# Optimization experiments

Measured on AMD Instinct MI355X. Metric: run time of the kernel, lower is better.

## Reference

```python
import jax, jax.numpy as jnp
import numpy as np

TEMPERATURE = 0.5
EPS = 1e-12  # F.normalize eps


def setup_inputs() -> dict:
    key = jax.random.key(0)
    z = jax.random.normal(key, (2048, 8, 256), dtype=jnp.float32)
    return {"z": z}


def reference(z):
    B, D = z.shape[0], z.shape[1]
    z = z.reshape(B, D, -1)  # [B, D, F]
    # F.normalize along features
    norm = jnp.linalg.norm(z, axis=-1, keepdims=True)
    zn = z / jnp.maximum(norm, EPS)

    # Positive term: per sample b, sim among D views -> [B, D, D], off-diagonal sum
    sim_pos = jnp.exp(jnp.einsum('bdf,bef->bde', zn, zn) / TEMPERATURE)
    eye_d = jnp.eye(D, dtype=bool)
    pos = jnp.sum(jnp.where(eye_d[None], 0.0, sim_pos), axis=(1, 2))  # [B]

    # Negative term: per view d, sim among B samples -> [D, B, B], row-wise off-diag mean, summed over views
    sim_neg = jnp.exp(jnp.einsum('bdf,cdf->dbc', zn, zn) / TEMPERATURE)
    eye_b = jnp.eye(B, dtype=bool)
    neg = jnp.sum(jnp.where(eye_b[None], 0.0, sim_neg), axis=-1) / (B - 1)  # [D, B]
    neg = jnp.sum(neg, axis=0)  # [B]

    logits = pos / (pos + neg)  # [B]
    # torch CrossEntropyLoss(reduction='sum') with 1-D input [C] and float target ones(C):
    # loss = -sum_c target_c * log_softmax(logits)_c = -sum(log_softmax(logits))
    error = -jnp.sum(jax.nn.log_softmax(logits))
    return error / B
```

## Files before the change

### kernel.cpp

```cpp
#include <hip/hip_runtime.h>
#include <hip/hip_bf16.h>

#define B_N 2048
#define D_V 8
#define F_D 256
#define TILE 128
#define BC 64
#define LSTR 264

#define SCALE_F 1.69864364f

#if defined(__has_builtin)
#  if __has_builtin(__builtin_amdgcn_exp2f)
#    define EXP2F(x) __builtin_amdgcn_exp2f(x)
#  else
#    define EXP2F(x) exp2f(x)
#  endif
#else
#  define EXP2F(x) exp2f(x)
#endif

typedef __attribute__((ext_vector_type(8))) short short8;
typedef __attribute__((ext_vector_type(4))) float floatx4;

__device__ inline unsigned short f2bf(float f) {
    __hip_bfloat16 h = __float2bfloat16(f);
    return *reinterpret_cast<unsigned short*>(&h);
}

__device__ inline float wave_reduce_sum(float v) {
    #pragma unroll
    for (int off = 1; off < 64; off <<= 1)
        v += __shfl_xor(v, off, 64);
    return v;
}

__global__ void norm_kernel(const float* __restrict__ z,
                            unsigned short* __restrict__ zn,
                            float* __restrict__ ns8) {
    int gid = blockIdx.x * blockDim.x + threadIdx.x;
    if (gid < D_V * B_N) ns8[gid] = 0.0f;
    int wave = gid >> 6;
    int lane = threadIdx.x & 63;
    const float4* zp = (const float4*)(z + (size_t)wave * F_D);
    float4 v = zp[lane];
    float ss = v.x * v.x + v.y * v.y + v.z * v.z + v.w * v.w;
    ss = wave_reduce_sum(ss);
    float inv = SCALE_F / fmaxf(sqrtf(ss), 1e-12f);
    int b = wave >> 3, d = wave & 7;
    unsigned short* op = zn + (size_t)d * (B_N * F_D) + (size_t)b * F_D + lane * 4;
    ushort4 o;
    o.x = f2bf(v.x * inv);
    o.y = f2bf(v.y * inv);
    o.z = f2bf(v.z * inv);
    o.w = f2bf(v.w * inv);
    *(ushort4*)op = o;
}

__global__ void pos_kernel(const unsigned short* __restrict__ zn,
                           float* __restrict__ pos) {
    int gw = (blockIdx.x * blockDim.x + threadIdx.x) >> 6;
    int lane = threadIdx.x & 63;
    int q = lane >> 4, li = lane & 15;
    int s0 = gw * 2;
    int b = s0 + (li >> 3), d = li & 7;
    const unsigned short* rowp = zn + (size_t)d * (B_N * F_D) + (size_t)b * F_D;
    short8 a[8];
    #pragma unroll
    for (int kk = 0; kk < 8; kk++)
        a[kk] = *(const short8*)(rowp + kk * 32 + q * 8);
    floatx4 acc = {0.f, 0.f, 0.f, 0.f};
    #pragma unroll
    for (int kk = 0; kk < 8; kk++)
        acc = __builtin_amdgcn_mfma_f32_16x16x32_bf16(a[kk], a[kk], acc, 0, 0, 0);
    float p0 = 0.f, p1 = 0.f;
    #pragma unroll
    for (int r = 0; r < 4; r++) {
        int row = q * 4 + r, col = li;
        bool same_sample = (row >> 3) == (col >> 3);
        if (same_sample && row != col) {
            float e = EXP2F(acc[r]);
            if (row < 8) p0 += e; else p1 += e;
        }
    }
    p0 = wave_reduce_sum(p0);
    p1 = wave_reduce_sum(p1);
    if (lane == 0) { pos[s0] = p0; pos[s0 + 1] = p1; }
}

__global__ __launch_bounds__(256)
void neg_kernel(const unsigned short* __restrict__ zn,
                float* __restrict__ ns8) {
    __shared__ __align__(16) unsigned short Bs[BC * LSTR];
    const int bid = blockIdx.x;
    const int d = bid & 7;
    int trem = bid >> 3;
    int i = 0;
    while (trem >= 16 - i) { trem -= 16 - i; ++i; }
    const int j = i + trem;
    const bool diag = (i == j);
    const unsigned short* Z = zn + (size_t)d * (B_N * F_D);
    int tid = threadIdx.x, w = tid >> 6, lane = tid & 63;
    int q = lane >> 4, li = lane & 15;
    int r0 = i * TILE + w * 32;

    short8 a[2][8];
    #pragma unroll
    for (int s = 0; s < 2; s++)
        #pragma unroll
        for (int kk = 0; kk < 8; kk++)
            a[s][kk] = *(const short8*)(Z + (size_t)(r0 + s * 16 + li) * F_D + kk * 32 + q * 8);

    float rs[2][4];
    #pragma unroll
    for (int s = 0; s < 2; s++)
        #pragma unroll
        for (int r = 0; r < 4; r++) rs[s][r] = 0.f;
    float cs[8];

    #pragma unroll
    for (int stage = 0; stage < 2; ++stage) {
        int c0 = j * TILE + stage * BC;
        __syncthreads();
        #pragma unroll
        for (int it = 0; it < 8; ++it) {
            int idx = it * 256 + tid;
            int row = idx >> 5, kc = idx & 31;
            *(short8*)(&Bs[row * LSTR + kc * 8]) =
                *(const short8*)(Z + (size_t)(c0 + row) * F_D + kc * 8);
        }
        __syncthreads();
        #pragma unroll
        for (int ct = 0; ct < 4; ++ct) {
            const unsigned short* bp = &Bs[(ct * 16 + li) * LSTR + q * 8];
            floatx4 acc[2];
            acc[0] = (floatx4){0.f, 0.f, 0.f, 0.f};
            acc[1] = (floatx4){0.f, 0.f, 0.f, 0.f};
            #pragma unroll
            for (int kk = 0; kk < 8; kk++) {
                short8 bf = *(const short8*)(bp + kk * 32);
                acc[0] = __builtin_amdgcn_mfma_f32_16x16x32_bf16(a[0][kk], bf, acc[0], 0, 0, 0);
                acc[1] = __builtin_amdgcn_mfma_f32_16x16x32_bf16(a[1][kk], bf, acc[1], 0, 0, 0);
            }
            int gcol = c0 + ct * 16 + li;
            float csum = 0.f;
            #pragma unroll
            for (int s = 0; s < 2; s++) {
                #pragma unroll
                for (int r = 0; r < 4; r++) {
                    float e = EXP2F(acc[s][r]);
                    if (diag) {
                        int grow = r0 + s * 16 + q * 4 + r;
                        if (grow == gcol) e = 0.f;
                    }
                    rs[s][r] += e;
                    csum += e;
                }
            }
            cs[stage * 4 + ct] = csum;
        }
    }

    #pragma unroll
    for (int off = 1; off < 16; off <<= 1)
        #pragma unroll
        for (int s = 0; s < 2; s++)
            #pragma unroll
            for (int r = 0; r < 4; r++)
                rs[s][r] += __shfl_xor(rs[s][r], off, 64);
    {
        float rv = 0.f;
        #pragma unroll
        for (int s = 0; s < 2; s++)
            #pragma unroll
            for (int r = 0; r < 4; r++)
                if (li == s * 4 + r) rv = rs[s][r];
        if (li < 8)
            atomicAdd(&ns8[d * B_N + r0 + (li >> 2) * 16 + q * 4 + (li & 3)], rv);
    }

    if (!diag) {
        #pragma unroll
        for (int c = 0; c < 8; c++) {
            cs[c] += __shfl_xor(cs[c], 16, 64);
            cs[c] += __shfl_xor(cs[c], 32, 64);
        }
        float v0 = 0.f, v1 = 0.f;
        #pragma unroll
        for (int c = 0; c < 4; c++)
            if (q == c) { v0 = cs[c]; v1 = cs[c + 4]; }
        atomicAdd(&ns8[d * B_N + j * TILE + q * 16 + li], v0);
        atomicAdd(&ns8[d * B_N + j * TILE + 64 + q * 16 + li], v1);
    }
}

__global__ void final_kernel(const float* __restrict__ pos,
                             const float* __restrict__ ns8,
                             float* __restrict__ out) {
    __shared__ float red[256];
    int t = threadIdx.x;
    float vals[8];
    float lmax = -1e30f;
    #pragma unroll
    for (int i = 0; i < 8; i++) {
        int idx = t * 8 + i;
        float nsum = 0.f;
        #pragma unroll
        for (int d = 0; d < D_V; d++) nsum += ns8[d * B_N + idx];
        float p = pos[idx];
        float n = nsum * (1.0f / (float)(B_N - 1));
        float l = p / (p + n);
        vals[i] = l;
        lmax = fmaxf(lmax, l);
    }
    red[t] = lmax; __syncthreads();
    for (int s = 128; s > 0; s >>= 1) {
        if (t < s) red[t] = fmaxf(red[t], red[t + s]);
        __syncthreads();
    }
    float m = red[0]; __syncthreads();
    float se = 0.f, sl = 0.f;
    #pragma unroll
    for (int i = 0; i < 8; i++) { se += expf(vals[i] - m); sl += vals[i]; }
    red[t] = se; __syncthreads();
    for (int s = 128; s > 0; s >>= 1) {
        if (t < s) red[t] += red[t + s];
        __syncthreads();
    }
    float S = red[0]; __syncthreads();
    red[t] = sl; __syncthreads();
    for (int s = 128; s > 0; s >>= 1) {
        if (t < s) red[t] += red[t + s];
        __syncthreads();
    }
    if (t == 0) out[0] = m + logf(S) - red[0] / (float)B_N;
}

extern "C" void kernel_launch(void* const* d_in, const int* in_sizes, int n_in,
                              void* d_out, int out_size, void* d_ws, size_t ws_size,
                              hipStream_t stream) {
    const float* z = (const float*)d_in[0];
    float* out = (float*)d_out;
    unsigned short* zn = (unsigned short*)d_ws;
    float* ns8 = (float*)((char*)d_ws + (size_t)D_V * B_N * F_D * 2);
    float* pos = ns8 + D_V * B_N;

    norm_kernel<<<dim3(4096), 256, 0, stream>>>(z, zn, ns8);
    pos_kernel<<<dim3(256), 256, 0, stream>>>(zn, pos);
    neg_kernel<<<dim3(136 * 8), 256, 0, stream>>>(zn, ns8);
    final_kernel<<<1, 256, 0, stream>>>(pos, ns8, out);
}
```

Baseline: 95.09 us.

## Fuse norm and pos kernels, double-buffer neg B tiles, use wave reductions in final

Merges the normalization and positive-term kernels into one launch: each block normalizes 4 samples, stages the bf16 rows in LDS and computes the per-sample view similarities from there, which removes a launch and a global re-read. The negative kernel now streams B columns in four 32-row chunks through a register-prefetched, double-buffered LDS tile, overlapping global loads with MFMA work. It also reduces column sums on the fly and sets launch bounds to 4 blocks per SM. The final reduction swaps shared-memory tree loops for wave shuffles, at the cost of more sync points per chunk in the neg kernel.

```diff
diff --git a/kernel.cpp b/kernel.cpp
--- a/kernel.cpp
+++ b/kernel.cpp
@@ -5,7 +5,7 @@
 #define D_V 8
 #define F_D 256
 #define TILE 128
-#define BC 64
+#define BC 32
 #define LSTR 264
 
 #define SCALE_F 1.69864364f
@@ -35,63 +35,74 @@
     return v;
 }
 
-__global__ void norm_kernel(const float* __restrict__ z,
-                            unsigned short* __restrict__ zn,
-                            float* __restrict__ ns8) {
-    int gid = blockIdx.x * blockDim.x + threadIdx.x;
+__device__ inline float wave_reduce_max(float v) {
+    #pragma unroll
+    for (int off = 1; off < 64; off <<= 1)
+        v = fmaxf(v, __shfl_xor(v, off, 64));
+    return v;
+}
+
+__global__ __launch_bounds__(256)
+void np_kernel(const float* __restrict__ z, unsigned short* __restrict__ zn,
+               float* __restrict__ ns8, float* __restrict__ pos) {
+    __shared__ __align__(16) unsigned short Zs[32 * LSTR];
+    int tid = threadIdx.x;
+    int gid = blockIdx.x * 256 + tid;
     if (gid < D_V * B_N) ns8[gid] = 0.0f;
-    int wave = gid >> 6;
-    int lane = threadIdx.x & 63;
-    const float4* zp = (const float4*)(z + (size_t)wave * F_D);
-    float4 v = zp[lane];
-    float ss = v.x * v.x + v.y * v.y + v.z * v.z + v.w * v.w;
-    ss = wave_reduce_sum(ss);
-    float inv = SCALE_F / fmaxf(sqrtf(ss), 1e-12f);
-    int b = wave >> 3, d = wave & 7;
-    unsigned short* op = zn + (size_t)d * (B_N * F_D) + (size_t)b * F_D + lane * 4;
-    ushort4 o;
-    o.x = f2bf(v.x * inv);
-    o.y = f2bf(v.y * inv);
-    o.z = f2bf(v.z * inv);
-    o.w = f2bf(v.w * inv);
-    *(ushort4*)op = o;
-}
-
-__global__ void pos_kernel(const unsigned short* __restrict__ zn,
-                           float* __restrict__ pos) {
-    int gw = (blockIdx.x * blockDim.x + threadIdx.x) >> 6;
-    int lane = threadIdx.x & 63;
-    int q = lane >> 4, li = lane & 15;
-    int s0 = gw * 2;
-    int b = s0 + (li >> 3), d = li & 7;
-    const unsigned short* rowp = zn + (size_t)d * (B_N * F_D) + (size_t)b * F_D;
-    short8 a[8];
-    #pragma unroll
-    for (int kk = 0; kk < 8; kk++)
-        a[kk] = *(const short8*)(rowp + kk * 32 + q * 8);
-    floatx4 acc = {0.f, 0.f, 0.f, 0.f};
-    #pragma unroll
-    for (int kk = 0; kk < 8; kk++)
-        acc = __builtin_amdgcn_mfma_f32_16x16x32_bf16(a[kk], a[kk], acc, 0, 0, 0);
-    float p0 = 0.f, p1 = 0.f;
-    #pragma unroll
-    for (int r = 0; r < 4; r++) {
-        int row = q * 4 + r, col = li;
-        bool same_sample = (row >> 3) == (col >> 3);
-        if (same_sample && row != col) {
-            float e = EXP2F(acc[r]);
-            if (row < 8) p0 += e; else p1 += e;
-        }
-    }
-    p0 = wave_reduce_sum(p0);
-    p1 = wave_reduce_sum(p1);
-    if (lane == 0) { pos[s0] = p0; pos[s0 + 1] = p1; }
-}
-
-__global__ __launch_bounds__(256)
+
+    int w = tid >> 6, lane = tid & 63;
+    int b = blockIdx.x * 4 + w;
+    #pragma unroll
+    for (int k = 0; k < 8; k++) {
+        const float4 v = ((const float4*)(z + ((size_t)b * 8 + k) * F_D))[lane];
+        float ss = v.x * v.x + v.y * v.y + v.z * v.z + v.w * v.w;
+        ss = wave_reduce_sum(ss);
+        float inv = SCALE_F / fmaxf(sqrtf(ss), 1e-12f);
+        ushort4 o;
+        o.x = f2bf(v.x * inv);
+        o.y = f2bf(v.y * inv);
+        o.z = f2bf(v.z * inv);
+        o.w = f2bf(v.w * inv);
+        ((ushort4*)(zn + (size_t)k * (B_N * F_D) + (size_t)b * F_D))[lane] = o;
+        *(ushort4*)(&Zs[(w * 8 + k) * LSTR + lane * 4]) = o;
+    }
+    __syncthreads();
+
+    if (w < 2) {
+        int q = lane >> 4, li = lane & 15;
+        int lr = (w * 2 + (li >> 3)) * 8 + (li & 7);
+        short8 a[8];
+        #pragma unroll
+        for (int kk = 0; kk < 8; kk++)
+            a[kk] = *(const short8*)(&Zs[lr * LSTR + kk * 32 + q * 8]);
+        floatx4 acc = {0.f, 0.f, 0.f, 0.f};
+        #pragma unroll
+        for (int kk = 0; kk < 8; kk++)
+            acc = __builtin_amdgcn_mfma_f32_16x16x32_bf16(a[kk], a[kk], acc, 0, 0, 0);
+        float p0 = 0.f, p1 = 0.f;
+        #pragma unroll
+        for (int r = 0; r < 4; r++) {
+            int row = q * 4 + r, col = li;
+            bool same_sample = (row >> 3) == (col >> 3);
+            if (same_sample && row != col) {
+                float e = EXP2F(acc[r]);
+                if (row < 8) p0 += e; else p1 += e;
+            }
+        }
+        p0 = wave_reduce_sum(p0);
+        p1 = wave_reduce_sum(p1);
+        if (lane == 0) {
+            int s0 = blockIdx.x * 4 + w * 2;
+            pos[s0] = p0;
+            pos[s0 + 1] = p1;
+        }
+    }
+}
+
+__global__ __launch_bounds__(256, 4)
 void neg_kernel(const unsigned short* __restrict__ zn,
                 float* __restrict__ ns8) {
-    __shared__ __align__(16) unsigned short Bs[BC * LSTR];
+    __shared__ __align__(16) unsigned short Bs[2][BC * LSTR];
     const int bid = blockIdx.x;
     const int d = bid & 7;
     int trem = bid >> 3;
@@ -103,6 +114,7 @@
     int tid = threadIdx.x, w = tid >> 6, lane = tid & 63;
     int q = lane >> 4, li = lane & 15;
     int r0 = i * TILE + w * 32;
+    const int jc = j * TILE;
 
     short8 a[2][8];
     #pragma unroll
@@ -111,28 +123,40 @@
         for (int kk = 0; kk < 8; kk++)
             a[s][kk] = *(const short8*)(Z + (size_t)(r0 + s * 16 + li) * F_D + kk * 32 + q * 8);
 
+    short8 breg[4];
+    #pragma unroll
+    for (int it = 0; it < 4; ++it) {
+        int idx = it * 256 + tid;
+        int row = idx >> 5, kc = idx & 31;
+        breg[it] = *(const short8*)(Z + (size_t)(jc + row) * F_D + kc * 8);
+    }
+    #pragma unroll
+    for (int it = 0; it < 4; ++it) {
+        int idx = it * 256 + tid;
+        int row = idx >> 5, kc = idx & 31;
+        *(short8*)(&Bs[0][row * LSTR + kc * 8]) = breg[it];
+    }
+    #pragma unroll
+    for (int it = 0; it < 4; ++it) {
+        int idx = it * 256 + tid;
+        int row = idx >> 5, kc = idx & 31;
+        breg[it] = *(const short8*)(Z + (size_t)(jc + BC + row) * F_D + kc * 8);
+    }
+
     float rs[2][4];
     #pragma unroll
     for (int s = 0; s < 2; s++)
         #pragma unroll
         for (int r = 0; r < 4; r++) rs[s][r] = 0.f;
-    float cs[8];
-
-    #pragma unroll
-    for (int stage = 0; stage < 2; ++stage) {
-        int c0 = j * TILE + stage * BC;
-        __syncthreads();
-        #pragma unroll
-        for (int it = 0; it < 8; ++it) {
-            int idx = it * 256 + tid;
-            int row = idx >> 5, kc = idx & 31;
-            *(short8*)(&Bs[row * LSTR + kc * 8]) =
-                *(const short8*)(Z + (size_t)(c0 + row) * F_D + kc * 8);
-        }
-        __syncthreads();
-        #pragma unroll
-        for (int ct = 0; ct < 4; ++ct) {
-            const unsigned short* bp = &Bs[(ct * 16 + li) * LSTR + q * 8];
+    float cacc[2] = {0.f, 0.f};
+
+    __syncthreads();
+
+    #pragma unroll
+    for (int st = 0; st < 4; ++st) {
+        #pragma unroll
+        for (int ct = 0; ct < 2; ++ct) {
+            const unsigned short* bp = &Bs[st & 1][(ct * 16 + li) * LSTR + q * 8];
             floatx4 acc[2];
             acc[0] = (floatx4){0.f, 0.f, 0.f, 0.f};
             acc[1] = (floatx4){0.f, 0.f, 0.f, 0.f};
@@ -142,7 +166,7 @@
                 acc[0] = __builtin_amdgcn_mfma_f32_16x16x32_bf16(a[0][kk], bf, acc[0], 0, 0, 0);
                 acc[1] = __builtin_amdgcn_mfma_f32_16x16x32_bf16(a[1][kk], bf, acc[1], 0, 0, 0);
             }
-            int gcol = c0 + ct * 16 + li;
+            int gcol = jc + st * BC + ct * 16 + li;
             float csum = 0.f;
             #pragma unroll
             for (int s = 0; s < 2; s++) {
@@ -157,8 +181,28 @@
                     csum += e;
                 }
             }
-            cs[stage * 4 + ct] = csum;
-        }
+            csum += __shfl_xor(csum, 16, 64);
+            csum += __shfl_xor(csum, 32, 64);
+            const int g = st * 2 + ct;
+            if (q == (g & 3)) cacc[g >> 2] += csum;
+        }
+        if (st < 3) {
+            #pragma unroll
+            for (int it = 0; it < 4; ++it) {
+                int idx = it * 256 + tid;
+                int row = idx >> 5, kc = idx & 31;
+                *(short8*)(&Bs[(st + 1) & 1][row * LSTR + kc * 8]) = breg[it];
+            }
+        }
+        if (st < 2) {
+            #pragma unroll
+            for (int it = 0; it < 4; ++it) {
+                int idx = it * 256 + tid;
+                int row = idx >> 5, kc = idx & 31;
+                breg[it] = *(const short8*)(Z + (size_t)(jc + (st + 2) * BC + row) * F_D + kc * 8);
+            }
+        }
+        __syncthreads();
     }
 
     #pragma unroll
@@ -180,25 +224,16 @@
     }
 
     if (!diag) {
-        #pragma unroll
-        for (int c = 0; c < 8; c++) {
-            cs[c] += __shfl_xor(cs[c], 16, 64);
-            cs[c] += __shfl_xor(cs[c], 32, 64);
-        }
-        float v0 = 0.f, v1 = 0.f;
-        #pragma unroll
-        for (int c = 0; c < 4; c++)
-            if (q == c) { v0 = cs[c]; v1 = cs[c + 4]; }
-        atomicAdd(&ns8[d * B_N + j * TILE + q * 16 + li], v0);
-        atomicAdd(&ns8[d * B_N + j * TILE + 64 + q * 16 + li], v1);
+        atomicAdd(&ns8[d * B_N + jc + q * 16 + li], cacc[0]);
+        atomicAdd(&ns8[d * B_N + jc + 64 + q * 16 + li], cacc[1]);
     }
 }
 
 __global__ void final_kernel(const float* __restrict__ pos,
                              const float* __restrict__ ns8,
                              float* __restrict__ out) {
-    __shared__ float red[256];
-    int t = threadIdx.x;
+    __shared__ float redm[4], reds[4], redl[4];
+    int t = threadIdx.x, w = t >> 6, lane = t & 63;
     float vals[8];
     float lmax = -1e30f;
     #pragma unroll
@@ -208,32 +243,26 @@
         #pragma unroll
         for (int d = 0; d < D_V; d++) nsum += ns8[d * B_N + idx];
         float p = pos[idx];
-        float n = nsum * (1.0f / (float)(B_N - 1));
-        float l = p / (p + n);
+        float l = p / (p + nsum * (1.0f / (float)(B_N - 1)));
         vals[i] = l;
         lmax = fmaxf(lmax, l);
     }
-    red[t] = lmax; __syncthreads();
-    for (int s = 128; s > 0; s >>= 1) {
-        if (t < s) red[t] = fmaxf(red[t], red[t + s]);
-        __syncthreads();
-    }
-    float m = red[0]; __syncthreads();
+    lmax = wave_reduce_max(lmax);
+    if (lane == 0) redm[w] = lmax;
+    __syncthreads();
+    float m = fmaxf(fmaxf(redm[0], redm[1]), fmaxf(redm[2], redm[3]));
     float se = 0.f, sl = 0.f;
     #pragma unroll
     for (int i = 0; i < 8; i++) { se += expf(vals[i] - m); sl += vals[i]; }
-    red[t] = se; __syncthreads();
-    for (int s = 128; s > 0; s >>= 1) {
-        if (t < s) red[t] += red[t + s];
-        __syncthreads();
-    }
-    float S = red[0]; __syncthreads();
-    red[t] = sl; __syncthreads();
-    for (int s = 128; s > 0; s >>= 1) {
-        if (t < s) red[t] += red[t + s];
-        __syncthreads();
-    }
-    if (t == 0) out[0] = m + logf(S) - red[0] / (float)B_N;
+    se = wave_reduce_sum(se);
+    sl = wave_reduce_sum(sl);
+    if (lane == 0) { reds[w] = se; redl[w] = sl; }
+    __syncthreads();
+    if (t == 0) {
+        float S = reds[0] + reds[1] + reds[2] + reds[3];
+        float L = redl[0] + redl[1] + redl[2] + redl[3];
+        out[0] = m + logf(S) - L * (1.0f / (float)B_N);
+    }
 }
 
 extern "C" void kernel_launch(void* const* d_in, const int* in_sizes, int n_in,
@@ -245,8 +274,7 @@
     float* ns8 = (float*)((char*)d_ws + (size_t)D_V * B_N * F_D * 2);
     float* pos = ns8 + D_V * B_N;
 
-    norm_kernel<<<dim3(4096), 256, 0, stream>>>(z, zn, ns8);
-    pos_kernel<<<dim3(256), 256, 0, stream>>>(zn, pos);
+    np_kernel<<<dim3(512), 256, 0, stream>>>(z, zn, ns8, pos);
     neg_kernel<<<dim3(136 * 8), 256, 0, stream>>>(zn, ns8);
     final_kernel<<<1, 256, 0, stream>>>(pos, ns8, out);
 }
```

Result: slower. 102.9 us (+8.2%).
